# Kernel tuning notes

Hardware: AMD Instinct MI355X
Metric: run time of the kernel (lower is better)

## Reference

```python
import jax, jax.numpy as jnp
import numpy as np

B, S, E, H = 2, 2048, 2048, 16
D = E // H  # head dim = 128
NEG = -1000000000.0


def setup_inputs() -> dict:
    key = jax.random.key(0)
    kx, kq, kk, kv, ko = jax.random.split(key, 5)
    scale = 1.0 / np.sqrt(E)
    return {
        "x": jax.random.normal(kx, (B, S, E), dtype=jnp.float32),
        "Wq": jax.random.normal(kq, (E, E), dtype=jnp.float32) * scale,
        "Wk": jax.random.normal(kk, (E, E), dtype=jnp.float32) * scale,
        "Wv": jax.random.normal(kv, (E, E), dtype=jnp.float32) * scale,
        "Wo": jax.random.normal(ko, (E, E), dtype=jnp.float32) * scale,
    }


def reference(x, Wq, Wk, Wv, Wo):
    # Linear(E,E,bias=False): y = x @ W.T
    q = jnp.einsum('bse,fe->bsf', x, Wq).reshape(B, S, H, D).transpose(0, 2, 1, 3)
    k = jnp.einsum('bse,fe->bsf', x, Wk).reshape(B, S, H, D).transpose(0, 2, 1, 3)
    v = jnp.einsum('bse,fe->bsf', x, Wv).reshape(B, S, H, D).transpose(0, 2, 1, 3)
    # causal additive mask: -1e9 above the diagonal
    mask = jnp.triu(jnp.full((S, S), NEG, dtype=x.dtype), k=1)
    scores = jnp.einsum('bhqd,bhkd->bhqk', q, k) / np.sqrt(D) + mask
    attn = jax.nn.softmax(scores, axis=-1)  # dropout=0.0 (eval)
    out = jnp.einsum('bhqk,bhkd->bhqd', attn, v)
    out = out.transpose(0, 2, 1, 3).reshape(B, S, E)
    return jnp.einsum('bse,fe->bsf', out, Wo)
```

## Files before the change

### kernel.cpp

```cpp
#include <hip/hip_runtime.h>
#include <hip/hip_bf16.h>
#include <stdint.h>

typedef __hip_bfloat16 bf16;
typedef __attribute__((ext_vector_type(8))) short bf16x8;
typedef __attribute__((ext_vector_type(4))) float f32x4;

#define MFMA16 __builtin_amdgcn_mfma_f32_16x16x32_bf16

__device__ __forceinline__ void gll16(const bf16* g, const bf16* l) {
    __builtin_amdgcn_global_load_lds(
        (const __attribute__((address_space(1))) void*)g,
        (__attribute__((address_space(3))) void*)(bf16*)l, 16, 0, 0);
}

__device__ __forceinline__ short f2b(float x) {
    bf16 h = __float2bfloat16(x);
    return *reinterpret_cast<short*>(&h);
}
__device__ __forceinline__ float b2f(short s) {
    union { uint32_t u; float f; } cv;
    cv.u = ((uint32_t)(uint16_t)s) << 16;
    return cv.f;
}

__global__ void cvt4(const float* __restrict__ x,  const float* __restrict__ wq,
                     const float* __restrict__ wk, const float* __restrict__ wv,
                     bf16* __restrict__ xb, bf16* __restrict__ w1,
                     bf16* __restrict__ w2, bf16* __restrict__ w3)
{
    int b = blockIdx.x;
    const float* s; bf16* d; int base;
    if      (b < 4096) { s = x;  d = xb; base = b; }
    else if (b < 6144) { s = wq; d = w1; base = b - 4096; }
    else if (b < 8192) { s = wk; d = w2; base = b - 6144; }
    else               { s = wv; d = w3; base = b - 8192; }
    int i = base * 2048 + threadIdx.x * 8;
    float4 a = *(const float4*)(s + i);
    float4 c = *(const float4*)(s + i + 4);
    bf16x8 v;
    v[0] = f2b(a.x); v[1] = f2b(a.y); v[2] = f2b(a.z); v[3] = f2b(a.w);
    v[4] = f2b(c.x); v[5] = f2b(c.y); v[6] = f2b(c.z); v[7] = f2b(c.w);
    *(bf16x8*)(d + i) = v;
}
__global__ void cvt1(const float* __restrict__ s, bf16* __restrict__ d) {
    int i = blockIdx.x * 2048 + threadIdx.x * 8;
    float4 a = *(const float4*)(s + i);
    float4 c = *(const float4*)(s + i + 4);
    bf16x8 v;
    v[0] = f2b(a.x); v[1] = f2b(a.y); v[2] = f2b(a.z); v[3] = f2b(a.w);
    v[4] = f2b(c.x); v[5] = f2b(c.y); v[6] = f2b(c.z); v[7] = f2b(c.w);
    *(bf16x8*)(d + i) = v;
}

__device__ __forceinline__ void gemm_core(const bf16* __restrict__ A,
                                          const bf16* __restrict__ Bw, int K,
                                          int m0, int n0,
                                          bf16* As, bf16* Bs, f32x4 acc[4][4])
{
    const int t    = threadIdx.x;
    const int wave = t >> 6;
    const int lane = t & 63;
    const int lr   = lane & 15;
    const int lq   = lane >> 4;
    const int wm   = (wave >> 1) * 64;
    const int wn   = (wave & 1) * 64;
    const int r8   = lane >> 3;
    const int c8   = lane & 7;
    const int gly  = ((c8 ^ r8) << 3);

    const bf16* Ag = A  + (size_t)(m0 + wave * 32 + r8) * K + gly;
    const bf16* Bg = Bw + (size_t)(n0 + wave * 32 + r8) * K + gly;
    bf16* AsW = As + wave * 32 * 64;
    bf16* BsW = Bs + wave * 32 * 64;
    const int sw0 = ((lq ^ (lr & 7)) << 3);
    const int sw1 = (((4 + lq) ^ (lr & 7)) << 3);

    for (int k0 = 0; k0 < K; k0 += 64) {
        __syncthreads();
#pragma unroll
        for (int c = 0; c < 4; ++c) {
            gll16(Ag + (size_t)(c * 8) * K + k0, AsW + c * 512);
            gll16(Bg + (size_t)(c * 8) * K + k0, BsW + c * 512);
        }
        __syncthreads();
#pragma unroll
        for (int kk = 0; kk < 2; ++kk) {
            const int sw = kk ? sw1 : sw0;
            bf16x8 af[4], bfr[4];
#pragma unroll
            for (int i = 0; i < 4; ++i)
                af[i] = *(const bf16x8*)(&As[(wm + i * 16 + lr) * 64 + sw]);
#pragma unroll
            for (int j = 0; j < 4; ++j)
                bfr[j] = *(const bf16x8*)(&Bs[(wn + j * 16 + lr) * 64 + sw]);
#pragma unroll
            for (int i = 0; i < 4; ++i)
#pragma unroll
                for (int j = 0; j < 4; ++j)
                    acc[i][j] = MFMA16(af[i], bfr[j], acc[i][j], 0, 0, 0);
        }
    }
}

__global__ __launch_bounds__(256, 2)
void gemm_qkv(const bf16* __restrict__ A,
              const bf16* __restrict__ Wq, const bf16* __restrict__ Wk,
              const bf16* __restrict__ Wv,
              bf16* __restrict__ Qo, bf16* __restrict__ Ko, bf16* __restrict__ Vo)
{
    __shared__ bf16 As[128 * 64];
    __shared__ bf16 Bs[128 * 64];
    const int sel = blockIdx.y >> 4;
    const int n0  = (blockIdx.y & 15) * 128;
    const int m0  = blockIdx.x * 128;
    const bf16* Bw = sel == 0 ? Wq : sel == 1 ? Wk : Wv;
    bf16* Cv = sel == 0 ? Qo : sel == 1 ? Ko : Vo;

    f32x4 acc[4][4];
#pragma unroll
    for (int i = 0; i < 4; ++i)
#pragma unroll
        for (int j = 0; j < 4; ++j) acc[i][j] = (f32x4)0.0f;

    gemm_core(A, Bw, 2048, m0, n0, As, Bs, acc);

    const int t = threadIdx.x, wave = t >> 6, lane = t & 63;
    const int lr = lane & 15, lq = lane >> 4;
    const int wm = (wave >> 1) * 64, wn = (wave & 1) * 64;
#pragma unroll
    for (int i = 0; i < 4; ++i) {
        const int mb = m0 + wm + i * 16 + lq * 4;
#pragma unroll
        for (int j = 0; j < 4; ++j) {
            const int n = n0 + wn + j * 16 + lr;
            const int h_ = n >> 7, d_ = n & 127;
            if (sel == 2) {
                const int b_ = mb >> 11, s_ = mb & 2047;
                bf16 pk[4];
#pragma unroll
                for (int r = 0; r < 4; ++r) pk[r] = __float2bfloat16(acc[i][j][r]);
                *(uint2*)(Cv + (size_t)(((b_ << 4) + h_) * 128 + d_) * 2048 + s_) =
                    *(const uint2*)pk;
            } else {
#pragma unroll
                for (int r = 0; r < 4; ++r) {
                    const int m = mb + r;
                    const int b_ = m >> 11, s_ = m & 2047;
                    Cv[(size_t)(((b_ << 4) + h_) * 2048 + s_) * 128 + d_] =
                        __float2bfloat16(acc[i][j][r]);
                }
            }
        }
    }
}

__global__ __launch_bounds__(256, 2)
void gemm_o(const bf16* __restrict__ A, const bf16* __restrict__ Bw,
            float* __restrict__ C, int N)
{
    __shared__ bf16 As[128 * 64];
    __shared__ bf16 Bs[128 * 64];
    const int m0 = blockIdx.x * 128;
    const int n0 = blockIdx.y * 128;

    f32x4 acc[4][4];
#pragma unroll
    for (int i = 0; i < 4; ++i)
#pragma unroll
        for (int j = 0; j < 4; ++j) acc[i][j] = (f32x4)0.0f;

    gemm_core(A, Bw, 2048, m0, n0, As, Bs, acc);

    const int t = threadIdx.x, wave = t >> 6, lane = t & 63;
    const int lr = lane & 15, lq = lane >> 4;
    const int wm = (wave >> 1) * 64, wn = (wave & 1) * 64;
#pragma unroll
    for (int i = 0; i < 4; ++i) {
        const int mb = m0 + wm + i * 16 + lq * 4;
#pragma unroll
        for (int j = 0; j < 4; ++j) {
            const int n = n0 + wn + j * 16 + lr;
#pragma unroll
            for (int r = 0; r < 4; ++r)
                C[(size_t)(mb + r) * N + n] = acc[i][j][r];
        }
    }
}

__global__ __launch_bounds__(512, 4)
void attn_fwd(const bf16* __restrict__ Q, const bf16* __restrict__ K,
              const bf16* __restrict__ V, bf16* __restrict__ O)
{
    __shared__ bf16 smem[40960];
    bf16* KsB0 = smem;
    bf16* KsB1 = smem + 8192;
    bf16* VsB0 = smem + 16384;
    bf16* VsB1 = smem + 24576;
    bf16* Pb   = smem + 32768;

    const int t    = threadIdx.x;
    const int wave = t >> 6;
    const int lane = t & 63;
    const int lr   = lane & 15;
    const int lq   = lane >> 4;

    const int bid  = blockIdx.x;
    const int half = bid >> 8;
    const int idx  = bid & 255;
    const int bh   = idx & 31;
    const int qtl  = idx >> 5;
    const int qt   = half ? (15 - qtl) : qtl;

    const int bhS = bh * 2048;
    const int q0  = qt * 128;
    const int q_g = q0 + wave * 16 + lr;

    const float scale = 0.08838834764831845f;
    const float L2E   = 1.4426950408889634f;
    const float SC    = scale * L2E;

    bf16x8 aq[4];
    {
        const bf16* qp = Q + (size_t)(bhS + q_g) * 128 + lq * 8;
#pragma unroll
        for (int ks = 0; ks < 4; ++ks) {
            bf16x8 v = *(const bf16x8*)(qp + ks * 32);
#pragma unroll
            for (int e = 0; e < 8; ++e)
                v[e] = f2b(b2f(v[e]) * SC);
            aq[ks] = v;
        }
    }

    const bf16* Kp0 = K + (size_t)(bhS + wave * 8 + (lane >> 4)) * 128
                        + (((lane & 15) ^ (lane >> 4)) << 3);
    const bf16* Kp1 = K + (size_t)(bhS + wave * 8 + 4 + (lane >> 4)) * 128
                        + (((lane & 15) ^ (4 + (lane >> 4))) << 3);
    const bf16* Vp0 = V + (size_t)(bh * 128 + wave * 16 + (lane >> 3)) * 2048
                        + (((lane & 7) ^ (lane >> 3)) << 3);

    int swz[4];
#pragma unroll
    for (int ks = 0; ks < 4; ++ks) swz[ks] = (((ks * 4 + lq) ^ (lr & 7)) << 3);
    int pw[4];
#pragma unroll
    for (int j = 0; j < 4; ++j)
        pw[j] = ((((j * 2) + (lq >> 1)) ^ (lr & 7)) << 3) + ((lq & 1) << 2);
    bf16* PbRow = Pb + (wave * 16 + lr) * 64;

    f32x4 acc_o[8];
#pragma unroll
    for (int i = 0; i < 8; ++i) acc_o[i] = (f32x4)0.0f;
    float mrow = -INFINITY, lrow = 0.0f;

    const int nkv = 2 * (qt + 1);
    {
        gll16(Kp0, KsB0 + wave * 1024);
        gll16(Kp1, KsB0 + wave * 1024 + 512);
        gll16(Vp0, VsB0 + wave * 1024);
        gll16(Vp0 + 8 * 2048, VsB0 + wave * 1024 + 512);
    }

    for (int tile = 0; tile < nkv; ++tile) {
        __syncthreads();
        const int cur = tile & 1;
        const bf16* KsC = cur ? KsB1 : KsB0;
        const bf16* VsC = cur ? VsB1 : VsB0;
        if (tile + 1 < nkv) {
            bf16* Kd = (cur ? KsB0 : KsB1) + wave * 1024;
            bf16* Vd = (cur ? VsB0 : VsB1) + wave * 1024;
            const size_t ko = (size_t)(tile + 1) * 64 * 128;
            const int    vo = (tile + 1) * 64;
            gll16(Kp0 + ko, Kd);
            gll16(Kp1 + ko, Kd + 512);
            gll16(Vp0 + vo, Vd);
            gll16(Vp0 + 8 * 2048 + vo, Vd + 512);
        }

        f32x4 acc_s[4];
#pragma unroll
        for (int j = 0; j < 4; ++j) acc_s[j] = (f32x4)0.0f;
#pragma unroll
        for (int ks = 0; ks < 4; ++ks) {
#pragma unroll
            for (int j = 0; j < 4; ++j) {
                bf16x8 ak = *(const bf16x8*)(&KsC[(j * 16 + lr) * 128 + swz[ks]]);
                acc_s[j] = MFMA16(ak, aq[ks], acc_s[j], 0, 0, 0);
            }
        }

        const int kv0 = tile * 64;
        if (kv0 + 63 > q0 + wave * 16) {
#pragma unroll
            for (int j = 0; j < 4; ++j)
#pragma unroll
                for (int r = 0; r < 4; ++r) {
                    const int kvg = kv0 + j * 16 + lq * 4 + r;
                    if (kvg > q_g) acc_s[j][r] = -1e30f;
                }
        }
        float mx = -1e30f;
#pragma unroll
        for (int j = 0; j < 4; ++j)
#pragma unroll
            for (int r = 0; r < 4; ++r) mx = fmaxf(mx, acc_s[j][r]);
        mx = fmaxf(mx, __shfl_xor(mx, 16));
        mx = fmaxf(mx, __shfl_xor(mx, 32));
        const float mnew  = fmaxf(mrow, mx);
        const float alpha = exp2f(mrow - mnew);
        mrow = mnew;

        float rs = 0.0f;
#pragma unroll
        for (int j = 0; j < 4; ++j) {
            bf16 pk[4];
#pragma unroll
            for (int r = 0; r < 4; ++r) {
                float p = exp2f(acc_s[j][r] - mnew);
                rs += p;
                pk[r] = __float2bfloat16(p);
            }
            *(uint2*)(PbRow + pw[j]) = *(const uint2*)pk;
        }
        rs += __shfl_xor(rs, 16);
        rs += __shfl_xor(rs, 32);
        lrow = lrow * alpha + rs;
#pragma unroll
        for (int i = 0; i < 8; ++i)
#pragma unroll
            for (int r = 0; r < 4; ++r) acc_o[i][r] *= alpha;

#pragma unroll
        for (int ks = 0; ks < 2; ++ks) {
            bf16x8 bp = *(const bf16x8*)(PbRow + swz[ks]);
#pragma unroll
            for (int i = 0; i < 8; ++i) {
                bf16x8 av = *(const bf16x8*)(&VsC[(i * 16 + lr) * 64 + swz[ks]]);
                acc_o[i] = MFMA16(av, bp, acc_o[i], 0, 0, 0);
            }
        }
    }

    __syncthreads();
    const float inv = 1.0f / lrow;
    bf16* OtW = smem + wave * 16 * 136;
#pragma unroll
    for (int i = 0; i < 8; ++i) {
        bf16 pk[4];
#pragma unroll
        for (int r = 0; r < 4; ++r) pk[r] = __float2bfloat16(acc_o[i][r] * inv);
        *(uint2*)(OtW + lr * 136 + i * 16 + lq * 4) = *(const uint2*)pk;
    }
    __builtin_amdgcn_s_waitcnt(0);
    const int b_ = bh >> 4, h_ = bh & 15;
    const int ro = lane >> 2;
    const int dc = (lane & 3) * 32;
    const bf16* src = OtW + ro * 136 + dc;
    bf16* dst = O + (size_t)(b_ * 2048 + q0 + wave * 16 + ro) * 2048 + h_ * 128 + dc;
#pragma unroll
    for (int u = 0; u < 4; ++u)
        *(uint4*)(dst + u * 8) = *(const uint4*)(src + u * 8);
}

extern "C" void kernel_launch(void* const* d_in, const int* in_sizes, int n_in,
                              void* d_out, int out_size, void* d_ws, size_t ws_size,
                              hipStream_t stream)
{
    const float* x  = (const float*)d_in[0];
    const float* Wq = (const float*)d_in[1];
    const float* Wk = (const float*)d_in[2];
    const float* Wv = (const float*)d_in[3];
    const float* Wo = (const float*)d_in[4];
    float* out = (float*)d_out;

    const size_t NX = 8388608;
    const size_t NW = 4194304;
    bf16* Xb = (bf16*)d_ws;
    bf16* W1 = Xb + NX;
    bf16* W2 = W1 + NW;
    bf16* W3 = W2 + NW;
    bf16* Qb = W3 + NW;
    bf16* Kb = Qb + NX;
    bf16* Vb = Kb + NX;
    bf16* AO = Xb;

    cvt4<<<dim3(10240), dim3(256), 0, stream>>>(x, Wq, Wk, Wv, Xb, W1, W2, W3);
    gemm_qkv<<<dim3(32, 48), dim3(256), 0, stream>>>(Xb, W1, W2, W3, Qb, Kb, Vb);
    cvt1<<<dim3(2048), dim3(256), 0, stream>>>(Wo, W1);
    attn_fwd<<<dim3(512), dim3(512), 0, stream>>>(Qb, Kb, Vb, AO);
    gemm_o<<<dim3(32, 16), dim3(256), 0, stream>>>(AO, W1, out, 2048);
}
```

Before: 343.5 us.

## Process two query row groups per wave in attention, halving block size

The attention kernel now runs 4 waves of 256 threads per block instead of 8, and each wave handles 32 query rows as two 16-row groups. Every K and V fragment read from LDS therefore feeds two MFMAs, which halves LDS read traffic per unit of math. Each wave also issues twice as many global-to-LDS loads per tile. The cost is doubled accumulator and register pressure per wave and fewer waves per block, which may reduce latency hiding. Launch bounds change to match.

```diff
diff --git a/kernel.cpp b/kernel.cpp
--- a/kernel.cpp
+++ b/kernel.cpp
@@ -188,16 +188,16 @@
     }
 }
 
-__global__ __launch_bounds__(512, 4)
+__global__ __launch_bounds__(256, 2)
 void attn_fwd(const bf16* __restrict__ Q, const bf16* __restrict__ K,
               const bf16* __restrict__ V, bf16* __restrict__ O)
 {
     __shared__ bf16 smem[40960];
-    bf16* KsB0 = smem;
-    bf16* KsB1 = smem + 8192;
-    bf16* VsB0 = smem + 16384;
-    bf16* VsB1 = smem + 24576;
-    bf16* Pb   = smem + 32768;
+    bf16* Ks0 = smem;
+    bf16* Ks1 = smem + 8192;
+    bf16* Vs0 = smem + 16384;
+    bf16* Vs1 = smem + 24576;
+    bf16* Pb  = smem + 32768;
 
     const int t    = threadIdx.x;
     const int wave = t >> 6;
@@ -212,33 +212,37 @@
     const int qtl  = idx >> 5;
     const int qt   = half ? (15 - qtl) : qtl;
 
-    const int bhS = bh * 2048;
-    const int q0  = qt * 128;
-    const int q_g = q0 + wave * 16 + lr;
+    const int bhS   = bh * 2048;
+    const int q0    = qt * 128;
+    const int qbase = q0 + wave * 32;
 
     const float scale = 0.08838834764831845f;
     const float L2E   = 1.4426950408889634f;
     const float SC    = scale * L2E;
 
-    bf16x8 aq[4];
-    {
-        const bf16* qp = Q + (size_t)(bhS + q_g) * 128 + lq * 8;
+    bf16x8 aq[2][4];
+#pragma unroll
+    for (int g = 0; g < 2; ++g) {
+        const bf16* qp = Q + (size_t)(bhS + qbase + g * 16 + lr) * 128 + lq * 8;
 #pragma unroll
         for (int ks = 0; ks < 4; ++ks) {
             bf16x8 v = *(const bf16x8*)(qp + ks * 32);
 #pragma unroll
-            for (int e = 0; e < 8; ++e)
-                v[e] = f2b(b2f(v[e]) * SC);
-            aq[ks] = v;
-        }
-    }
-
-    const bf16* Kp0 = K + (size_t)(bhS + wave * 8 + (lane >> 4)) * 128
-                        + (((lane & 15) ^ (lane >> 4)) << 3);
-    const bf16* Kp1 = K + (size_t)(bhS + wave * 8 + 4 + (lane >> 4)) * 128
-                        + (((lane & 15) ^ (4 + (lane >> 4))) << 3);
-    const bf16* Vp0 = V + (size_t)(bh * 128 + wave * 16 + (lane >> 3)) * 2048
-                        + (((lane & 7) ^ (lane >> 3)) << 3);
+            for (int e = 0; e < 8; ++e) v[e] = f2b(b2f(v[e]) * SC);
+            aq[g][ks] = v;
+        }
+    }
+
+    const int krr = lane >> 4;
+    int swk[4];
+    const bf16* Kp[4];
+#pragma unroll
+    for (int c = 0; c < 4; ++c) {
+        swk[c] = (((lane & 15) ^ ((c * 4 + krr) & 7)) << 3);
+        Kp[c] = K + (size_t)(bhS + wave * 16 + c * 4 + krr) * 128 + swk[c];
+    }
+    const bf16* Vp = V + (size_t)(bh * 128 + wave * 32 + (lane >> 3)) * 2048
+                       + (((lane & 7) ^ (lane >> 3)) << 3);
 
     int swz[4];
 #pragma unroll
@@ -247,119 +251,142 @@
 #pragma unroll
     for (int j = 0; j < 4; ++j)
         pw[j] = ((((j * 2) + (lq >> 1)) ^ (lr & 7)) << 3) + ((lq & 1) << 2);
-    bf16* PbRow = Pb + (wave * 16 + lr) * 64;
-
-    f32x4 acc_o[8];
-#pragma unroll
-    for (int i = 0; i < 8; ++i) acc_o[i] = (f32x4)0.0f;
-    float mrow = -INFINITY, lrow = 0.0f;
+    bf16* PbW = Pb + wave * 2048;
+
+    f32x4 acc_o[2][8];
+#pragma unroll
+    for (int g = 0; g < 2; ++g)
+#pragma unroll
+        for (int i = 0; i < 8; ++i) acc_o[g][i] = (f32x4)0.0f;
+    float mrow[2] = {-INFINITY, -INFINITY}, lrow[2] = {0.0f, 0.0f};
 
     const int nkv = 2 * (qt + 1);
+
     {
-        gll16(Kp0, KsB0 + wave * 1024);
-        gll16(Kp1, KsB0 + wave * 1024 + 512);
-        gll16(Vp0, VsB0 + wave * 1024);
-        gll16(Vp0 + 8 * 2048, VsB0 + wave * 1024 + 512);
+        bf16* Kd = Ks0 + wave * 2048;
+        bf16* Vd = Vs0 + wave * 2048;
+#pragma unroll
+        for (int c = 0; c < 4; ++c) {
+            gll16(Kp[c], Kd + c * 512);
+            gll16(Vp + c * 16384, Vd + c * 512);
+        }
     }
 
     for (int tile = 0; tile < nkv; ++tile) {
         __syncthreads();
         const int cur = tile & 1;
-        const bf16* KsC = cur ? KsB1 : KsB0;
-        const bf16* VsC = cur ? VsB1 : VsB0;
+        const bf16* KsC = cur ? Ks1 : Ks0;
+        const bf16* VsC = cur ? Vs1 : Vs0;
         if (tile + 1 < nkv) {
-            bf16* Kd = (cur ? KsB0 : KsB1) + wave * 1024;
-            bf16* Vd = (cur ? VsB0 : VsB1) + wave * 1024;
-            const size_t ko = (size_t)(tile + 1) * 64 * 128;
+            bf16* Kd = (cur ? Ks0 : Ks1) + wave * 2048;
+            bf16* Vd = (cur ? Vs0 : Vs1) + wave * 2048;
+            const size_t ko = (size_t)(tile + 1) * 8192;
             const int    vo = (tile + 1) * 64;
-            gll16(Kp0 + ko, Kd);
-            gll16(Kp1 + ko, Kd + 512);
-            gll16(Vp0 + vo, Vd);
-            gll16(Vp0 + 8 * 2048 + vo, Vd + 512);
-        }
-
-        f32x4 acc_s[4];
-#pragma unroll
-        for (int j = 0; j < 4; ++j) acc_s[j] = (f32x4)0.0f;
+#pragma unroll
+            for (int c = 0; c < 4; ++c) {
+                gll16(Kp[c] + ko, Kd + c * 512);
+                gll16(Vp + c * 16384 + vo, Vd + c * 512);
+            }
+        }
+
+        f32x4 acc_s[2][4];
+#pragma unroll
+        for (int g = 0; g < 2; ++g)
+#pragma unroll
+            for (int j = 0; j < 4; ++j) acc_s[g][j] = (f32x4)0.0f;
 #pragma unroll
         for (int ks = 0; ks < 4; ++ks) {
 #pragma unroll
             for (int j = 0; j < 4; ++j) {
                 bf16x8 ak = *(const bf16x8*)(&KsC[(j * 16 + lr) * 128 + swz[ks]]);
-                acc_s[j] = MFMA16(ak, aq[ks], acc_s[j], 0, 0, 0);
+                acc_s[0][j] = MFMA16(ak, aq[0][ks], acc_s[0][j], 0, 0, 0);
+                acc_s[1][j] = MFMA16(ak, aq[1][ks], acc_s[1][j], 0, 0, 0);
             }
         }
 
         const int kv0 = tile * 64;
-        if (kv0 + 63 > q0 + wave * 16) {
+        if (kv0 + 63 > qbase) {
+#pragma unroll
+            for (int g = 0; g < 2; ++g) {
+                const int q_g = qbase + g * 16 + lr;
+#pragma unroll
+                for (int j = 0; j < 4; ++j)
+#pragma unroll
+                    for (int r = 0; r < 4; ++r) {
+                        const int kvg = kv0 + j * 16 + lq * 4 + r;
+                        if (kvg > q_g) acc_s[g][j][r] = -1e30f;
+                    }
+            }
+        }
+
+#pragma unroll
+        for (int g = 0; g < 2; ++g) {
+            float mx = -1e30f;
 #pragma unroll
             for (int j = 0; j < 4; ++j)
 #pragma unroll
+                for (int r = 0; r < 4; ++r) mx = fmaxf(mx, acc_s[g][j][r]);
+            mx = fmaxf(mx, __shfl_xor(mx, 16));
+            mx = fmaxf(mx, __shfl_xor(mx, 32));
+            const float mnew  = fmaxf(mrow[g], mx);
+            const float alpha = exp2f(mrow[g] - mnew);
+            mrow[g] = mnew;
+
+            float rs = 0.0f;
+#pragma unroll
+            for (int j = 0; j < 4; ++j) {
+                bf16 pk[4];
+#pragma unroll
                 for (int r = 0; r < 4; ++r) {
-                    const int kvg = kv0 + j * 16 + lq * 4 + r;
-                    if (kvg > q_g) acc_s[j][r] = -1e30f;
+                    float p = exp2f(acc_s[g][j][r] - mnew);
+                    rs += p;
+                    pk[r] = __float2bfloat16(p);
                 }
-        }
-        float mx = -1e30f;
-#pragma unroll
-        for (int j = 0; j < 4; ++j)
-#pragma unroll
-            for (int r = 0; r < 4; ++r) mx = fmaxf(mx, acc_s[j][r]);
-        mx = fmaxf(mx, __shfl_xor(mx, 16));
-        mx = fmaxf(mx, __shfl_xor(mx, 32));
-        const float mnew  = fmaxf(mrow, mx);
-        const float alpha = exp2f(mrow - mnew);
-        mrow = mnew;
-
-        float rs = 0.0f;
-#pragma unroll
-        for (int j = 0; j < 4; ++j) {
-            bf16 pk[4];
-#pragma unroll
-            for (int r = 0; r < 4; ++r) {
-                float p = exp2f(acc_s[j][r] - mnew);
-                rs += p;
-                pk[r] = __float2bfloat16(p);
-            }
-            *(uint2*)(PbRow + pw[j]) = *(const uint2*)pk;
-        }
-        rs += __shfl_xor(rs, 16);
-        rs += __shfl_xor(rs, 32);
-        lrow = lrow * alpha + rs;
-#pragma unroll
-        for (int i = 0; i < 8; ++i)
-#pragma unroll
-            for (int r = 0; r < 4; ++r) acc_o[i][r] *= alpha;
+                *(uint2*)(PbW + (g * 16 + lr) * 64 + pw[j]) = *(const uint2*)pk;
+            }
+            rs += __shfl_xor(rs, 16);
+            rs += __shfl_xor(rs, 32);
+            lrow[g] = lrow[g] * alpha + rs;
+#pragma unroll
+            for (int i = 0; i < 8; ++i)
+#pragma unroll
+                for (int r = 0; r < 4; ++r) acc_o[g][i][r] *= alpha;
+        }
 
 #pragma unroll
         for (int ks = 0; ks < 2; ++ks) {
-            bf16x8 bp = *(const bf16x8*)(PbRow + swz[ks]);
+            bf16x8 bp0 = *(const bf16x8*)(PbW + lr * 64 + swz[ks]);
+            bf16x8 bp1 = *(const bf16x8*)(PbW + (16 + lr) * 64 + swz[ks]);
 #pragma unroll
             for (int i = 0; i < 8; ++i) {
                 bf16x8 av = *(const bf16x8*)(&VsC[(i * 16 + lr) * 64 + swz[ks]]);
-                acc_o[i] = MFMA16(av, bp, acc_o[i], 0, 0, 0);
+                acc_o[0][i] = MFMA16(av, bp0, acc_o[0][i], 0, 0, 0);
+                acc_o[1][i] = MFMA16(av, bp1, acc_o[1][i], 0, 0, 0);
             }
         }
     }
 
     __syncthreads();
-    const float inv = 1.0f / lrow;
-    bf16* OtW = smem + wave * 16 * 136;
-#pragma unroll
-    for (int i = 0; i < 8; ++i) {
-        bf16 pk[4];
-#pragma unroll
-        for (int r = 0; r < 4; ++r) pk[r] = __float2bfloat16(acc_o[i][r] * inv);
-        *(uint2*)(OtW + lr * 136 + i * 16 + lq * 4) = *(const uint2*)pk;
+    bf16* OtW = smem + wave * 32 * 136;
+#pragma unroll
+    for (int g = 0; g < 2; ++g) {
+        const float inv = 1.0f / lrow[g];
+#pragma unroll
+        for (int i = 0; i < 8; ++i) {
+            bf16 pk[4];
+#pragma unroll
+            for (int r = 0; r < 4; ++r) pk[r] = __float2bfloat16(acc_o[g][i][r] * inv);
+            *(uint2*)(OtW + (g * 16 + lr) * 136 + i * 16 + lq * 4) = *(const uint2*)pk;
+        }
     }
     __builtin_amdgcn_s_waitcnt(0);
     const int b_ = bh >> 4, h_ = bh & 15;
-    const int ro = lane >> 2;
-    const int dc = (lane & 3) * 32;
+    const int ro = lane >> 1;
+    const int dc = (lane & 1) * 64;
     const bf16* src = OtW + ro * 136 + dc;
-    bf16* dst = O + (size_t)(b_ * 2048 + q0 + wave * 16 + ro) * 2048 + h_ * 128 + dc;
-#pragma unroll
-    for (int u = 0; u < 4; ++u)
+    bf16* dst = O + (size_t)(b_ * 2048 + q0 + wave * 32 + ro) * 2048 + h_ * 128 + dc;
+#pragma unroll
+    for (int u = 0; u < 8; ++u)
         *(uint4*)(dst + u * 8) = *(const uint4*)(src + u * 8);
 }
 
@@ -388,6 +415,6 @@
     cvt4<<<dim3(10240), dim3(256), 0, stream>>>(x, Wq, Wk, Wv, Xb, W1, W2, W3);
     gemm_qkv<<<dim3(32, 48), dim3(256), 0, stream>>>(Xb, W1, W2, W3, Qb, Kb, Vb);
     cvt1<<<dim3(2048), dim3(256), 0, stream>>>(Wo, W1);
-    attn_fwd<<<dim3(512), dim3(512), 0, stream>>>(Qb, Kb, Vb, AO);
+    attn_fwd<<<dim3(512), dim3(256), 0, stream>>>(Qb, Kb, Vb, AO);
     gemm_o<<<dim3(32, 16), dim3(256), 0, stream>>>(AO, W1, out, 2048);
 }
```

After: 352.1 us. 1.03x slower.
